# Kernel optimization log

Hardware: AMD Instinct MI355X
Metric: run time of the kernel (lower is better)

Reference implementation:

```python
import jax, jax.numpy as jnp
import numpy as np

BI, BC = 128, 128      # image batch, caption batch
NR, NW = 36, 50        # regions per image, words per caption
EMB = 1024             # joint embedding dim
MASK = -1.0            # fill value for invalid (region, word) pairs


def setup_inputs() -> dict:
    key = jax.random.key(0)
    k1, k2, k3, k4 = jax.random.split(key, 4)
    imgs = jax.random.normal(k1, (BI, NR, EMB), dtype=jnp.float32)
    caps = jax.random.normal(k2, (BC, NW, EMB), dtype=jnp.float32)
    # valid lengths in [1, NR] / [1, NW]; force max so shapes are static
    img_lens = jax.random.randint(k3, (BI,), 1, NR + 1).at[0].set(NR).astype(jnp.int32)
    cap_lens = jax.random.randint(k4, (BC,), 1, NW + 1).at[0].set(NW).astype(jnp.int32)
    return {"imgs": imgs, "caps": caps, "img_lens": img_lens, "cap_lens": cap_lens}


def reference(imgs, caps, img_lens, cap_lens):
    # all-pairs region-word similarities: [bi, bc, n_r, n_w]
    n_r, n_w = imgs.shape[1], caps.shape[1]
    sims = jnp.einsum('ire,cwe->icrw', imgs, caps)
    # torch source computes sims under @torch.no_grad()
    sims = jax.lax.stop_gradient(sims)
    mask_i = jnp.arange(n_r) < img_lens[:, None]   # [bi, n_r]
    mask_c = jnp.arange(n_w) < cap_lens[:, None]   # [bc, n_w]
    mask = mask_i[:, None, :, None] & mask_c[None, :, None, :]  # [bi, bc, n_r, n_w]
    sims = jnp.where(mask, sims, MASK)
    # max-pool over region dim -> [bi, bc, n_w]
    return sims.max(axis=2)
```

## Files before the change

### kernel.cpp

```cpp
#include <hip/hip_runtime.h>
#include <cstdint>

#define NBI 128
#define NBC 128
#define NR_ 36
#define NW_ 50
#define EMB_ 1024
#define MTOT (NBI * NR_)
#define NTOT (NBC * NW_)

typedef _Float16 f16;
typedef _Float16 f16x8 __attribute__((ext_vector_type(8)));
typedef float f32x4 __attribute__((ext_vector_type(4)));

__global__ void cvt_kernel(const float* __restrict__ srcA, f16* __restrict__ dstA, int nA8,
                           const float* __restrict__ srcB, f16* __restrict__ dstB, int nB8) {
  int i = blockIdx.x * 256 + threadIdx.x;
  const float* src;
  f16* dst;
  if (i < nA8) {
    src = srcA; dst = dstA;
  } else {
    i -= nA8;
    if (i >= nB8) return;
    src = srcB; dst = dstB;
  }
  const float4* s = (const float4*)src;
  float4 a = s[2 * i];
  float4 b = s[2 * i + 1];
  union { f16 h[8]; uint4 u; } r;
  r.h[0] = (f16)a.x; r.h[1] = (f16)a.y; r.h[2] = (f16)a.z; r.h[3] = (f16)a.w;
  r.h[4] = (f16)b.x; r.h[5] = (f16)b.y; r.h[6] = (f16)b.z; r.h[7] = (f16)b.w;
  ((uint4*)dst)[i] = r.u;
}

__launch_bounds__(256, 3)
__global__ void gemm_max_kernel(const f16* __restrict__ A, const f16* __restrict__ B,
                                const int* __restrict__ img_lens,
                                const int* __restrict__ cap_lens,
                                float* __restrict__ out) {
  __shared__ unsigned char smem[34816];

  const int bx = blockIdx.x;
  const int L = (bx & 7) * 200 + (bx >> 3);
  const int sc = L / 320;
  const int rem = L - sc * 320;
  const int bm = rem & 31;
  const int bn = sc * 10 + (rem >> 5);

  const int t = threadIdx.x;
  const int lane = t & 63;
  const int wv = t >> 6;

  f32x4 acc[9][2] = {};

  const char* Ab = (const char*)A + (size_t)(bm * 144) * 2048;
  const char* Bb = (const char*)B + (size_t)(bn * 128) * 2048;

  int sdstA[5], sgofA[5];
#pragma unroll
  for (int j = 0; j < 5; ++j) {
    int u = t + 256 * j;
    int row = u >> 3;
    int phys = (u & 7) * 16;
    int logical = phys ^ ((row & 7) << 4);
    sdstA[j] = u * 16;
    sgofA[j] = row * 2048 + logical;
  }
  int sdstB[4], sgofB[4];
#pragma unroll
  for (int j = 0; j < 4; ++j) {
    int u = t + 256 * j;
    int row = u >> 3;
    int phys = (u & 7) * 16;
    int logical = phys ^ ((row & 7) << 4);
    sdstB[j] = 18432 + u * 16;
    sgofB[j] = row * 2048 + logical;
  }

  for (int ck = 0; ck < 16; ++ck) {
    const int k0b = ck * 128;
#pragma unroll
    for (int j = 0; j < 4; ++j) {
      __builtin_amdgcn_global_load_lds(
          (const __attribute__((address_space(1))) void*)(Ab + (size_t)sgofA[j] + k0b),
          (__attribute__((address_space(3))) void*)(smem + sdstA[j]), 16, 0, 0);
    }
    if (t < 128) {
      __builtin_amdgcn_global_load_lds(
          (const __attribute__((address_space(1))) void*)(Ab + (size_t)sgofA[4] + k0b),
          (__attribute__((address_space(3))) void*)(smem + sdstA[4]), 16, 0, 0);
    }
#pragma unroll
    for (int j = 0; j < 4; ++j) {
      __builtin_amdgcn_global_load_lds(
          (const __attribute__((address_space(1))) void*)(Bb + (size_t)sgofB[j] + k0b),
          (__attribute__((address_space(3))) void*)(smem + sdstB[j]), 16, 0, 0);
    }
    __syncthreads();

#pragma unroll
    for (int kk = 0; kk < 2; ++kk) {
      f16x8 af[9], bf[2];
#pragma unroll
      for (int mt = 0; mt < 9; ++mt) {
        int row = mt * 16 + (lane & 15);
        int col = (kk * 64 + (lane >> 4) * 16) ^ ((row & 7) << 4);
        af[mt] = *(const f16x8*)(smem + row * 128 + col);
      }
#pragma unroll
      for (int nt = 0; nt < 2; ++nt) {
        int row = wv * 32 + nt * 16 + (lane & 15);
        int col = (kk * 64 + (lane >> 4) * 16) ^ ((row & 7) << 4);
        bf[nt] = *(const f16x8*)(smem + 18432 + row * 128 + col);
      }
#pragma unroll
      for (int mt = 0; mt < 9; ++mt)
#pragma unroll
        for (int nt = 0; nt < 2; ++nt)
          acc[mt][nt] = __builtin_amdgcn_mfma_f32_16x16x32_f16(af[mt], bf[nt], acc[mt][nt], 0, 0, 0);
    }
    __syncthreads();
  }

  const int q4 = ((lane >> 4) << 2);
  const int cg0 = bn * 128 + wv * 32 + (lane & 15);
  const int cg1 = cg0 + 16;
  const int c0 = cg0 / 50, w0 = cg0 - 50 * c0;
  const int c1 = cg1 / 50, w1 = cg1 - 50 * c1;
  const int cap0 = cap_lens[c0], cap1 = cap_lens[c1];

#pragma unroll
  for (int k = 0; k < 4; ++k) {
    const int gi = bm * 4 + k;
    const int len = img_lens[gi];
    const int lo = 36 * k, hi = 36 * k + len;
    float v0 = -3.0e38f, v1 = -3.0e38f;
#pragma unroll
    for (int mt = 0; mt < 9; ++mt) {
#pragma unroll
      for (int r4 = 0; r4 < 4; ++r4) {
        int row = mt * 16 + q4 + r4;
        if (row >= lo && row < hi) {
          v0 = fmaxf(v0, acc[mt][0][r4]);
          v1 = fmaxf(v1, acc[mt][1][r4]);
        }
      }
    }
    v0 = fmaxf(v0, __shfl_xor(v0, 16)); v0 = fmaxf(v0, __shfl_xor(v0, 32));
    v1 = fmaxf(v1, __shfl_xor(v1, 16)); v1 = fmaxf(v1, __shfl_xor(v1, 32));
    if (len < NR_) { v0 = fmaxf(v0, -1.0f); v1 = fmaxf(v1, -1.0f); }
    if (lane < 16) {
      float o0 = (w0 >= cap0) ? -1.0f : v0;
      float o1 = (w1 >= cap1) ? -1.0f : v1;
      out[(size_t)gi * 6400 + cg0] = o0;
      out[(size_t)gi * 6400 + cg1] = o1;
    }
  }
}

extern "C" void kernel_launch(void* const* d_in, const int* in_sizes, int n_in,
                              void* d_out, int out_size, void* d_ws, size_t ws_size,
                              hipStream_t stream) {
  const float* imgs = (const float*)d_in[0];
  const float* caps = (const float*)d_in[1];
  const int* img_lens = (const int*)d_in[2];
  const int* cap_lens = (const int*)d_in[3];
  float* out = (float*)d_out;

  char* ws = (char*)d_ws;
  f16* Af = (f16*)ws;
  f16* Bf = (f16*)(ws + (size_t)MTOT * EMB_ * 2);

  const int nA8 = MTOT * EMB_ / 8;
  const int nB8 = NTOT * EMB_ / 8;
  const int ncvt = nA8 + nB8;

  cvt_kernel<<<(ncvt + 255) / 256, 256, 0, stream>>>(imgs, Af, nA8, caps, Bf, nB8);
  gemm_max_kernel<<<32 * 50, 256, 0, stream>>>(Af, Bf, img_lens, cap_lens, out);
}
```

Baseline: 152.4 us.

## Pack valid regions and words densely to skip padded GEMM work

```diff
diff --git a/kernel.cpp b/kernel.cpp
--- a/kernel.cpp
+++ b/kernel.cpp
@@ -8,45 +8,121 @@
 #define EMB_ 1024
 #define MTOT (NBI * NR_)
 #define NTOT (NBC * NW_)
+#define OUTN (NBI * NBC * NW_)
+
+#define BM 144
+#define MAXMB 44
+#define ASLOTS (MAXMB * 144)
+#define MT_NMB 0
+#define MT_NNT 1
+#define MT_NCOL 2
+#define MT_IMGF 16
+#define MT_LO 64
+#define MT_ROWSRC 256
+#define MT_COLSRC (256 + ASLOTS)
+#define META_INTS (MT_COLSRC + NTOT)
 
 typedef _Float16 f16;
 typedef _Float16 f16x8 __attribute__((ext_vector_type(8)));
 typedef float f32x4 __attribute__((ext_vector_type(4)));
 
-__global__ void cvt_kernel(const float* __restrict__ srcA, f16* __restrict__ dstA, int nA8,
-                           const float* __restrict__ srcB, f16* __restrict__ dstB, int nB8) {
-  int i = blockIdx.x * 256 + threadIdx.x;
-  const float* src;
-  f16* dst;
-  if (i < nA8) {
-    src = srcA; dst = dstA;
+__global__ void plan_kernel(const int* __restrict__ img_lens, const int* __restrict__ cap_lens,
+                            int* __restrict__ meta) {
+  __shared__ int s_imgf[45], s_lo[128], s_blk[128], s_capstart[128], s_scal[3];
+  const int t = threadIdx.x;
+  if (t == 0) {
+    int nb = 0, used = 0;
+    s_imgf[0] = 0;
+    for (int i = 0; i < 128; ++i) {
+      int len = img_lens[i];
+      if (used + len > BM) { ++nb; s_imgf[nb] = i; used = 0; }
+      s_blk[i] = nb; s_lo[i] = used; used += len;
+    }
+    ++nb; 
+    for (int b = nb; b <= 44; ++b) s_imgf[b] = 128;
+    s_scal[0] = nb;
+    int nc = 0;
+    for (int c = 0; c < 128; ++c) { s_capstart[c] = nc; nc += cap_lens[c]; }
+    s_scal[1] = (nc + 127) >> 7;
+    s_scal[2] = nc;
+  }
+  __syncthreads();
+  if (t < 3) meta[MT_NMB + t] = s_scal[t];
+  if (t < 45) meta[MT_IMGF + t] = s_imgf[t];
+  if (t < 128) meta[MT_LO + t] = s_lo[t];
+  for (int k = t; k < ASLOTS; k += 256) meta[MT_ROWSRC + k] = -1;
+  for (int k = t; k < NTOT; k += 256) meta[MT_COLSRC + k] = -1;
+  __syncthreads();
+  if (t < 128) {
+    int len = img_lens[t];
+    int base = s_blk[t] * BM + s_lo[t];
+    for (int r = 0; r < len; ++r) meta[MT_ROWSRC + base + r] = t * 36 + r;
+    int cap = cap_lens[t];
+    int cbase = s_capstart[t];
+    for (int w = 0; w < cap; ++w) meta[MT_COLSRC + cbase + w] = t * 50 + w;
+  }
+}
+
+__global__ void prep_kernel(const float* __restrict__ imgs, const float* __restrict__ caps,
+                            const int* __restrict__ cap_lens, const int* __restrict__ meta,
+                            f16* __restrict__ Af, f16* __restrict__ Bf, float* __restrict__ out) {
+  int idx = blockIdx.x * 256 + threadIdx.x;
+  const int nA = ASLOTS * 128;
+  const int nB = NTOT * 128;
+  if (idx < nA) {
+    int row = idx >> 7, u = idx & 127;
+    int src = meta[MT_ROWSRC + row];
+    union { f16 h[8]; uint4 q; } r;
+    if (src >= 0) {
+      const float4* s = (const float4*)(imgs + (size_t)src * 1024 + u * 8);
+      float4 a = s[0], b = s[1];
+      r.h[0] = (f16)a.x; r.h[1] = (f16)a.y; r.h[2] = (f16)a.z; r.h[3] = (f16)a.w;
+      r.h[4] = (f16)b.x; r.h[5] = (f16)b.y; r.h[6] = (f16)b.z; r.h[7] = (f16)b.w;
+    } else {
+      r.q = uint4{0u, 0u, 0u, 0u};
+    }
+    ((uint4*)Af)[idx] = r.q;
+  } else if (idx < nA + nB) {
+    int k = idx - nA;
+    int row = k >> 7, u = k & 127;
+    int src = meta[MT_COLSRC + row];
+    union { f16 h[8]; uint4 q; } r;
+    if (src >= 0) {
+      const float4* s = (const float4*)(caps + (size_t)src * 1024 + u * 8);
+      float4 a = s[0], b = s[1];
+      r.h[0] = (f16)a.x; r.h[1] = (f16)a.y; r.h[2] = (f16)a.z; r.h[3] = (f16)a.w;
+      r.h[4] = (f16)b.x; r.h[5] = (f16)b.y; r.h[6] = (f16)b.z; r.h[7] = (f16)b.w;
+    } else {
+      r.q = uint4{0u, 0u, 0u, 0u};
+    }
+    ((uint4*)Bf)[idx - nA] = r.q;
   } else {
-    i -= nA8;
-    if (i >= nB8) return;
-    src = srcB; dst = dstB;
-  }
-  const float4* s = (const float4*)src;
-  float4 a = s[2 * i];
-  float4 b = s[2 * i + 1];
-  union { f16 h[8]; uint4 u; } r;
-  r.h[0] = (f16)a.x; r.h[1] = (f16)a.y; r.h[2] = (f16)a.z; r.h[3] = (f16)a.w;
-  r.h[4] = (f16)b.x; r.h[5] = (f16)b.y; r.h[6] = (f16)b.z; r.h[7] = (f16)b.w;
-  ((uint4*)dst)[i] = r.u;
+    int k = idx - nA - nB;
+    if (k < OUTN) {
+      int col = k % 6400;
+      int c = col / 50, w = col - 50 * c;
+      if (w >= cap_lens[c]) out[k] = -1.0f;
+    }
+  }
 }
 
 __launch_bounds__(256, 3)
 __global__ void gemm_max_kernel(const f16* __restrict__ A, const f16* __restrict__ B,
                                 const int* __restrict__ img_lens,
-                                const int* __restrict__ cap_lens,
+                                const int* __restrict__ meta,
                                 float* __restrict__ out) {
   __shared__ unsigned char smem[34816];
 
   const int bx = blockIdx.x;
-  const int L = (bx & 7) * 200 + (bx >> 3);
-  const int sc = L / 320;
-  const int rem = L - sc * 320;
-  const int bm = rem & 31;
-  const int bn = sc * 10 + (rem >> 5);
+  const int L = (bx & 7) * 275 + (bx >> 3);
+  const int sc = L / 440;
+  const int rem = L - sc * 440;
+  const int bm = rem % 44;
+  const int bn = sc * 10 + rem / 44;
+
+  const int n_mblks = meta[MT_NMB];
+  const int n_ntiles = meta[MT_NNT];
+  if (bm >= n_mblks || bn >= n_ntiles) return;
 
   const int t = threadIdx.x;
   const int lane = t & 63;
@@ -54,7 +130,7 @@
 
   f32x4 acc[9][2] = {};
 
-  const char* Ab = (const char*)A + (size_t)(bm * 144) * 2048;
+  const char* Ab = (const char*)A + (size_t)(bm * BM) * 2048;
   const char* Bb = (const char*)B + (size_t)(bn * 128) * 2048;
 
   int sdstA[5], sgofA[5];
@@ -126,15 +202,15 @@
   const int q4 = ((lane >> 4) << 2);
   const int cg0 = bn * 128 + wv * 32 + (lane & 15);
   const int cg1 = cg0 + 16;
-  const int c0 = cg0 / 50, w0 = cg0 - 50 * c0;
-  const int c1 = cg1 / 50, w1 = cg1 - 50 * c1;
-  const int cap0 = cap_lens[c0], cap1 = cap_lens[c1];
-
-#pragma unroll
-  for (int k = 0; k < 4; ++k) {
-    const int gi = bm * 4 + k;
-    const int len = img_lens[gi];
-    const int lo = 36 * k, hi = 36 * k + len;
+  int oc0 = -1, oc1 = -1;
+  if (lane < 16) { oc0 = meta[MT_COLSRC + cg0]; oc1 = meta[MT_COLSRC + cg1]; }
+
+  const int jf = meta[MT_IMGF + bm];
+  const int jl = meta[MT_IMGF + bm + 1];
+  for (int j = jf; j < jl; ++j) {
+    const int len = img_lens[j];
+    const int lo = meta[MT_LO + j];
+    const int hi = lo + len;
     float v0 = -3.0e38f, v1 = -3.0e38f;
 #pragma unroll
     for (int mt = 0; mt < 9; ++mt) {
@@ -151,10 +227,8 @@
     v1 = fmaxf(v1, __shfl_xor(v1, 16)); v1 = fmaxf(v1, __shfl_xor(v1, 32));
     if (len < NR_) { v0 = fmaxf(v0, -1.0f); v1 = fmaxf(v1, -1.0f); }
     if (lane < 16) {
-      float o0 = (w0 >= cap0) ? -1.0f : v0;
-      float o1 = (w1 >= cap1) ? -1.0f : v1;
-      out[(size_t)gi * 6400 + cg0] = o0;
-      out[(size_t)gi * 6400 + cg1] = o1;
+      if (oc0 >= 0) out[(size_t)j * 6400 + oc0] = v0;
+      if (oc1 >= 0) out[(size_t)j * 6400 + oc1] = v1;
     }
   }
 }
@@ -170,12 +244,14 @@
 
   char* ws = (char*)d_ws;
   f16* Af = (f16*)ws;
-  f16* Bf = (f16*)(ws + (size_t)MTOT * EMB_ * 2);
-
-  const int nA8 = MTOT * EMB_ / 8;
-  const int nB8 = NTOT * EMB_ / 8;
-  const int ncvt = nA8 + nB8;
-
-  cvt_kernel<<<(ncvt + 255) / 256, 256, 0, stream>>>(imgs, Af, nA8, caps, Bf, nB8);
-  gemm_max_kernel<<<32 * 50, 256, 0, stream>>>(Af, Bf, img_lens, cap_lens, out);
-}
+  f16* Bf = (f16*)(ws + (size_t)ASLOTS * EMB_ * 2);
+  int* meta = (int*)(ws + (size_t)ASLOTS * EMB_ * 2 + (size_t)NTOT * EMB_ * 2);
+
+  const int nA = ASLOTS * 128;
+  const int nB = NTOT * 128;
+  const int nprep = nA + nB + OUTN;
+
+  plan_kernel<<<1, 256, 0, stream>>>(img_lens, cap_lens, meta);
+  prep_kernel<<<(nprep + 255) / 256, 256, 0, stream>>>(imgs, caps, cap_lens, meta, Af, Bf, out);
+  gemm_max_kernel<<<MAXMB * 50, 256, 0, stream>>>(Af, Bf, img_lens, meta, out);
+}
```

After: 159.9 us. 1.05x slower.
